# Kernel tuning notes

Hardware: AMD Instinct MI355X
Metric: run time of the kernel (lower is better)

Reference implementation:

```python
import jax, jax.numpy as jnp
import numpy as np


def setup_inputs() -> dict:
    key = jax.random.key(0)
    ks = jax.random.split(key, 4)
    B, S, D, H, E = 2, 2048, 1024, 4096, 8
    scale_in = 1.0 / np.sqrt(D)
    scale_h = 1.0 / np.sqrt(H)
    return {
        "x": jax.random.normal(ks[0], (B, S, D), dtype=jnp.float32),
        "Wr": jax.random.normal(ks[1], (E, D), dtype=jnp.float32) * scale_in,
        "br": jnp.zeros((E,), dtype=jnp.float32),
        "W1": jax.random.normal(ks[2], (E, H, D), dtype=jnp.float32) * scale_in,
        "b1": jnp.zeros((E, H), dtype=jnp.float32),
        "W2": jax.random.normal(ks[3], (E, D, H), dtype=jnp.float32) * scale_h,
        "b2": jnp.zeros((E, D), dtype=jnp.float32),
        "top_k": 2,
    }


def reference(x, Wr, br, W1, b1, W2, b2, top_k):
    B, S, D = x.shape
    E = Wr.shape[0]
    x_flat = x.reshape(-1, D)                                   # [N, D]
    # Router: top-k logits, softmax over the selected k values only
    logits = x_flat @ Wr.T + br                                 # [N, E]
    top_vals, top_idx = jax.lax.top_k(logits, top_k)            # [N, k]
    gates = jax.nn.softmax(top_vals, axis=-1)                   # [N, k]
    # Per-expert combine weight: gate_e[n, e] = sum_k gates[n, k] * 1[top_idx[n,k]==e]
    gate_e = jnp.einsum("nk,nke->ne", gates,
                        jax.nn.one_hot(top_idx, E, dtype=x.dtype))  # [N, E]
    # Dense all-expert MLP (grouped GEMM), then masked combine. Same math as
    # the per-expert gather/scatter loop: unselected experts get zero gate.
    h = jax.nn.relu(jnp.einsum("nd,ehd->neh", x_flat, W1) + b1)     # [N, E, H]
    y = jnp.einsum("neh,edh->ned", h, W2) + b2                      # [N, E, D]
    out = jnp.einsum("ned,ne->nd", y, gate_e)                       # [N, D]
    return out.reshape(B, S, D)
```

## Files before the change

### kernel.cpp

```cpp
#include <hip/hip_runtime.h>
#include <hip/hip_bf16.h>
#include <stdint.h>

#define N_TOK 4096
#define D_ 1024
#define H_ 4096
#define E_ 8
#define NSLOT (N_TOK*2)
#define BM 128
#define BN 128
#define BK 32
#define MAXT 72

typedef __attribute__((ext_vector_type(8))) short short8;
typedef __attribute__((ext_vector_type(4))) float floatx4;
typedef unsigned int u32;

__device__ __forceinline__ unsigned short f2bf(float f){
    union { float f; unsigned int u; } c; c.f = f;
    unsigned int u = c.u;
    unsigned int r = (u + 0x7fffu + ((u >> 16) & 1u)) >> 16;
    return (unsigned short)r;
}

__device__ __forceinline__ void async16(const void* g, void* l){
    __builtin_amdgcn_global_load_lds(
        (const __attribute__((address_space(1))) u32*)g,
        (__attribute__((address_space(3))) u32*)l, 16, 0, 0);
}

__global__ __launch_bounds__(256) void cvt_kernel(
    const float* __restrict__ src, unsigned short* __restrict__ dst, int n4)
{
    int stride = gridDim.x * 256;
    for (int i = blockIdx.x * 256 + threadIdx.x; i < n4; i += stride){
        float4 v = ((const float4*)src)[i];
        ushort4 o; o.x=f2bf(v.x); o.y=f2bf(v.y); o.z=f2bf(v.z); o.w=f2bf(v.w);
        ((ushort4*)dst)[i] = o;
    }
}

__global__ __launch_bounds__(256) void router_kernel(
    const float* __restrict__ x, const float* __restrict__ Wr,
    const float* __restrict__ br, int* __restrict__ topIdx,
    float* __restrict__ topGate)
{
    int n = blockIdx.x * 4 + (threadIdx.x >> 6);
    int lane = threadIdx.x & 63;
    const float4* xp = (const float4*)(x + (size_t)n * D_);
    float acc[E_];
#pragma unroll
    for (int e = 0; e < E_; e++) acc[e] = 0.f;
#pragma unroll
    for (int j = 0; j < 4; j++){
        int idx = j * 64 + lane;
        float4 xv = xp[idx];
#pragma unroll
        for (int e = 0; e < E_; e++){
            float4 wv = ((const float4*)(Wr + (size_t)e * D_))[idx];
            acc[e] += xv.x*wv.x + xv.y*wv.y + xv.z*wv.z + xv.w*wv.w;
        }
    }
#pragma unroll
    for (int e = 0; e < E_; e++){
        float v = acc[e];
        for (int off = 32; off > 0; off >>= 1) v += __shfl_xor(v, off, 64);
        acc[e] = v;
    }
    if (lane == 0){
        float best = -1e30f, second = -1e30f; int bi = 0, si = 0;
#pragma unroll
        for (int e = 0; e < E_; e++){
            float v = acc[e] + br[e];
            if (v > best){ second = best; si = bi; best = v; bi = e; }
            else if (v > second){ second = v; si = e; }
        }
        float e1 = __expf(second - best);
        float denom = 1.f + e1;
        topIdx[n*2+0] = bi;  topIdx[n*2+1] = si;
        topGate[n*2+0] = 1.f/denom;  topGate[n*2+1] = e1/denom;
    }
}

__global__ __launch_bounds__(256) void hist_kernel(
    const int* __restrict__ topIdx, int* __restrict__ hdr)
{
    __shared__ int c[E_];
    int t = threadIdx.x;
    if (t < E_) c[t] = 0;
    __syncthreads();
    int e = topIdx[blockIdx.x * 256 + t];
    atomicAdd(&c[e], 1);
    __syncthreads();
    if (t < E_) hdr[256 + blockIdx.x * E_ + t] = c[t];
}

__global__ __launch_bounds__(64) void scan2_kernel(int* __restrict__ hdr)
{
    __shared__ int cnt[32 * E_];
    __shared__ int tot[E_];
    __shared__ int offs[E_ + 1];
    int t = threadIdx.x;
    for (int i = t; i < 32 * E_; i += 64) cnt[i] = hdr[256 + i];
    __syncthreads();
    if (t < E_){
        int s = 0;
        for (int b = 0; b < 32; b++) s += cnt[b * E_ + t];
        tot[t] = s;
    }
    __syncthreads();
    if (t == 0){
        int o = 0;
        for (int e = 0; e < E_; e++){ offs[e] = o; o += tot[e]; }
        offs[E_] = o;
    }
    __syncthreads();
    if (t < E_ + 1) hdr[16 + t] = offs[t];
    if (t < E_){
        int run = offs[t];
        for (int b = 0; b < 32; b++){ hdr[512 + b * E_ + t] = run; run += cnt[b * E_ + t]; }
    }
    if (t == 0){
        int tn = 0;
        for (int e = 0; e < E_; e++){
            int nt = (tot[e] + BM - 1) >> 7;
            for (int i = 0; i < nt; i++){ hdr[32 + tn] = e; hdr[112 + tn] = offs[e] + (i << 7); tn++; }
        }
        for (; tn < MAXT; tn++){ hdr[32 + tn] = -1; hdr[112 + tn] = 0; }
    }
}

__global__ __launch_bounds__(256) void pos_kernel(
    const int* __restrict__ topIdx, const float* __restrict__ topGate,
    const int* __restrict__ hdr, int* __restrict__ posOf,
    int* __restrict__ rowTok, float* __restrict__ rowGate)
{
    __shared__ int c[E_];
    int t = threadIdx.x;
    if (t < E_) c[t] = 0;
    __syncthreads();
    int slot = blockIdx.x * 256 + t;
    int e = topIdx[slot];
    int r = atomicAdd(&c[e], 1);
    int pos = hdr[512 + blockIdx.x * E_ + e] + r;
    posOf[slot] = pos;
    rowTok[pos] = slot >> 1;
    rowGate[pos] = topGate[slot];
}

__global__ __launch_bounds__(256) void copy_kernel(
    const float* __restrict__ x, const int* __restrict__ posOf,
    unsigned short* __restrict__ xg)
{
    int slot = blockIdx.x * 4 + (threadIdx.x >> 6);
    int lane = threadIdx.x & 63;
    int n = slot >> 1;
    int pos = posOf[slot];
    const float4* xp = (const float4*)(x + (size_t)n * D_);
    ushort4* op = (ushort4*)(xg + (size_t)pos * D_);
#pragma unroll
    for (int j = 0; j < 4; j++){
        float4 v = xp[j * 64 + lane];
        ushort4 o; o.x=f2bf(v.x); o.y=f2bf(v.y); o.z=f2bf(v.z); o.w=f2bf(v.w);
        op[j * 64 + lane] = o;
    }
}

template<int MODE, bool BF16B>
__global__ __launch_bounds__(256) void moe_gemm(
    const unsigned short* __restrict__ A, int Ktot,
    const void* __restrict__ Wbase, size_t wStride,
    const float* __restrict__ biasBase, int biasStride,
    const int* __restrict__ hdr,
    const int* __restrict__ rowTok, const float* __restrict__ rowGate,
    unsigned short* __restrict__ hout, float* __restrict__ out)
{
    int gid = blockIdx.y * gridDim.x + blockIdx.x;
    int per = gridDim.x * 8;
    int g = gid / per, rr = gid % per;
    int by = g * 8 + (rr & 7);
    int bx = rr >> 3;

    int e = hdr[32 + bx];
    if (e < 0) return;
    int rowBase = hdr[112 + bx];
    int validRows = hdr[16 + e + 1] - rowBase;

    int kChunk = Ktot / gridDim.z;
    int kStart = blockIdx.z * kChunk;

    __shared__ __align__(16) unsigned short As[BM * BK];
    __shared__ __align__(16) unsigned short BsH[BF16B ? BN * BK : 1];
    __shared__ __align__(16) float BsF[BF16B ? 1 : BN * BK];

    const float* biasE = biasBase + (size_t)e * biasStride + by * BN;

    const int tid  = threadIdx.x;
    const int lane = tid & 63, wave = tid >> 6;
    const int wm = wave & 1, wn = wave >> 1;
    const int l16 = lane & 15, quad = lane >> 4;

    floatx4 acc[4][4];
#pragma unroll
    for (int mi = 0; mi < 4; mi++)
#pragma unroll
        for (int ni = 0; ni < 4; ni++)
            acc[mi][ni] = (floatx4){0.f,0.f,0.f,0.f};

    int aS[2], aRow[2], aCol[2];
#pragma unroll
    for (int i = 0; i < 2; i++){
        int s = i * 256 + tid;
        aS[i] = s;
        int r = rowBase + (s >> 2);
        aRow[i] = r < (NSLOT - 1) ? r : (NSLOT - 1);
        aCol[i] = (s & 3) * 8;
    }

    if (BF16B){
        const unsigned short* Wexp = (const unsigned short*)Wbase
            + (size_t)e * wStride + (size_t)(by * BN) * Ktot;
        for (int k0 = kStart; k0 < kStart + kChunk; k0 += BK){
#pragma unroll
            for (int i = 0; i < 2; i++)
                async16(A + (size_t)aRow[i] * Ktot + k0 + aCol[i], (char*)As + aS[i] * 16);
#pragma unroll
            for (int i = 0; i < 2; i++){
                int s = i * 256 + tid;
                async16(Wexp + (size_t)(s >> 2) * Ktot + k0 + (s & 3) * 8,
                        (char*)BsH + s * 16);
            }
            __syncthreads();
            short8 af[4], bfr[4];
#pragma unroll
            for (int mi = 0; mi < 4; mi++)
                af[mi] = *(const short8*)(As + (wm*64 + mi*16 + l16) * BK + quad * 8);
#pragma unroll
            for (int ni = 0; ni < 4; ni++)
                bfr[ni] = *(const short8*)(BsH + (wn*64 + ni*16 + l16) * BK + quad * 8);
#pragma unroll
            for (int mi = 0; mi < 4; mi++)
#pragma unroll
                for (int ni = 0; ni < 4; ni++)
                    acc[mi][ni] = __builtin_amdgcn_mfma_f32_16x16x32_bf16(
                        af[mi], bfr[ni], acc[mi][ni], 0, 0, 0);
            __syncthreads();
        }
    } else {
        const float* Wexp = (const float*)Wbase
            + (size_t)e * wStride + (size_t)(by * BN) * Ktot;
        int bS[4], bRow[4], bCol[4];
#pragma unroll
        for (int i = 0; i < 4; i++){
            int s = i * 256 + tid;
            bS[i] = s;
            int r = s >> 3, c = s & 7;
            bRow[i] = r;
            bCol[i] = (c ^ (r & 7)) * 4;
        }
        for (int k0 = kStart; k0 < kStart + kChunk; k0 += BK){
#pragma unroll
            for (int i = 0; i < 2; i++)
                async16(A + (size_t)aRow[i] * Ktot + k0 + aCol[i], (char*)As + aS[i] * 16);
#pragma unroll
            for (int i = 0; i < 4; i++)
                async16(Wexp + (size_t)bRow[i] * Ktot + k0 + bCol[i], (char*)BsF + bS[i] * 16);
            __syncthreads();
            short8 af[4], bfr[4];
#pragma unroll
            for (int mi = 0; mi < 4; mi++)
                af[mi] = *(const short8*)(As + (wm*64 + mi*16 + l16) * BK + quad * 8);
#pragma unroll
            for (int ni = 0; ni < 4; ni++){
                int n = wn*64 + ni*16 + l16;
                int g0 = (2*quad)     ^ (n & 7);
                int g1 = (2*quad + 1) ^ (n & 7);
                float4 u0 = *(const float4*)(BsF + n * BK + g0 * 4);
                float4 u1 = *(const float4*)(BsF + n * BK + g1 * 4);
                union { short8 s; __hip_bfloat162 h[4]; } u;
                u.h[0] = __float22bfloat162_rn(make_float2(u0.x, u0.y));
                u.h[1] = __float22bfloat162_rn(make_float2(u0.z, u0.w));
                u.h[2] = __float22bfloat162_rn(make_float2(u1.x, u1.y));
                u.h[3] = __float22bfloat162_rn(make_float2(u1.z, u1.w));
                bfr[ni] = u.s;
            }
#pragma unroll
            for (int mi = 0; mi < 4; mi++)
#pragma unroll
                for (int ni = 0; ni < 4; ni++)
                    acc[mi][ni] = __builtin_amdgcn_mfma_f32_16x16x32_bf16(
                        af[mi], bfr[ni], acc[mi][ni], 0, 0, 0);
            __syncthreads();
        }
    }

    bool addB = (MODE == 1) || (blockIdx.z == 0);
#pragma unroll
    for (int mi = 0; mi < 4; mi++){
#pragma unroll
        for (int r = 0; r < 4; r++){
            int rl = wm*64 + mi*16 + quad*4 + r;
            if (rl >= validRows) continue;
            int grow = rowBase + rl;
            int   tok  = 0;
            float gate = 0.f;
            if (MODE == 2){ tok = rowTok[grow]; gate = rowGate[grow]; }
#pragma unroll
            for (int ni = 0; ni < 4; ni++){
                int lcol = wn*64 + ni*16 + l16;
                int gcol = by * BN + lcol;
                float v = acc[mi][ni][r] + (addB ? biasE[lcol] : 0.f);
                if (MODE == 1){
                    v = v > 0.f ? v : 0.f;
                    hout[(size_t)grow * H_ + gcol] = f2bf(v);
                } else {
                    atomicAdd(out + (size_t)tok * D_ + gcol, gate * v);
                }
            }
        }
    }
}

extern "C" void kernel_launch(void* const* d_in, const int* in_sizes, int n_in,
                              void* d_out, int out_size, void* d_ws, size_t ws_size,
                              hipStream_t stream)
{
    (void)in_sizes; (void)n_in;
    const float* x  = (const float*)d_in[0];
    const float* Wr = (const float*)d_in[1];
    const float* br = (const float*)d_in[2];
    const float* W1 = (const float*)d_in[3];
    const float* b1 = (const float*)d_in[4];
    const float* W2 = (const float*)d_in[5];
    const float* b2 = (const float*)d_in[6];
    float* out = (float*)d_out;

    char* ws = (char*)d_ws;
    int*   hdr     = (int*)ws;
    int*   topIdx  = (int*)  (ws + 4096);
    float* topGate = (float*)(ws + 36864);
    int*   posOf   = (int*)  (ws + 69632);
    int*   rowTok  = (int*)  (ws + 102400);
    float* rowGate = (float*)(ws + 135168);
    unsigned short* xg   = (unsigned short*)(ws + 262144);
    unsigned short* hbuf = (unsigned short*)(ws + 17039360);
    unsigned short* w1b  = (unsigned short*)(ws + 84148224);
    unsigned short* w2b  = (unsigned short*)(ws + 151257088);
    const bool full = ws_size >= 218365952ull;

    hipMemsetAsync(d_out, 0, (size_t)out_size * sizeof(float), stream);

    router_kernel<<<N_TOK/4, 256, 0, stream>>>(x, Wr, br, topIdx, topGate);
    hist_kernel<<<32, 256, 0, stream>>>(topIdx, hdr);
    scan2_kernel<<<1, 64, 0, stream>>>(hdr);
    pos_kernel<<<32, 256, 0, stream>>>(topIdx, topGate, hdr, posOf, rowTok, rowGate);
    copy_kernel<<<NSLOT/4, 256, 0, stream>>>(x, posOf, xg);

    if (full){
        cvt_kernel<<<2048, 256, 0, stream>>>(W1, w1b, (E_*H_*D_)/4);
        cvt_kernel<<<2048, 256, 0, stream>>>(W2, w2b, (E_*D_*H_)/4);
        moe_gemm<1,true><<<dim3(MAXT, H_/BN, 1), 256, 0, stream>>>(
            xg, D_, w1b, (size_t)H_ * D_, b1, H_, hdr, rowTok, rowGate, hbuf, nullptr);
        moe_gemm<2,true><<<dim3(MAXT, D_/BN, 2), 256, 0, stream>>>(
            hbuf, H_, w2b, (size_t)D_ * H_, b2, D_, hdr, rowTok, rowGate, nullptr, out);
    } else {
        moe_gemm<1,false><<<dim3(MAXT, H_/BN, 1), 256, 0, stream>>>(
            xg, D_, W1, (size_t)H_ * D_, b1, H_, hdr, rowTok, rowGate, hbuf, nullptr);
        moe_gemm<2,false><<<dim3(MAXT, D_/BN, 2), 256, 0, stream>>>(
            hbuf, H_, W2, (size_t)D_ * H_, b2, D_, hdr, rowTok, rowGate, nullptr, out);
    }
}
```

Baseline: 664.4 us.

## Double-buffer bf16 GEMM LDS tiles and XOR-swizzle chunks to avoid bank conflicts

The bf16-weight GEMM path now keeps two LDS stages for the A and B tiles. The next k-slice is prefetched with async global-to-LDS copies while the MFMAs run on the current slice, and only one barrier per iteration remains. The 16-byte chunk position inside each row is also XOR-swizzled by row bits, applied on both store and load, to cut LDS bank conflicts on the short8 fragment reads. This doubles the LDS footprint of that path, which may lower occupancy, and the fp32-weight path is left unpipelined.

```diff
diff --git a/kernel.cpp b/kernel.cpp
--- a/kernel.cpp
+++ b/kernel.cpp
@@ -189,8 +189,8 @@
     int kChunk = Ktot / gridDim.z;
     int kStart = blockIdx.z * kChunk;
 
-    __shared__ __align__(16) unsigned short As[BM * BK];
-    __shared__ __align__(16) unsigned short BsH[BF16B ? BN * BK : 1];
+    __shared__ __align__(16) unsigned short As[2][BM * BK];
+    __shared__ __align__(16) unsigned short BsH[BF16B ? 2 * BN * BK : 1];
     __shared__ __align__(16) float BsF[BF16B ? 1 : BN * BK];
 
     const float* biasE = biasBase + (size_t)e * biasStride + by * BN;
@@ -207,48 +207,74 @@
         for (int ni = 0; ni < 4; ni++)
             acc[mi][ni] = (floatx4){0.f,0.f,0.f,0.f};
 
-    int aS[2], aRow[2], aCol[2];
-#pragma unroll
-    for (int i = 0; i < 2; i++){
-        int s = i * 256 + tid;
-        aS[i] = s;
-        int r = rowBase + (s >> 2);
-        aRow[i] = r < (NSLOT - 1) ? r : (NSLOT - 1);
-        aCol[i] = (s & 3) * 8;
-    }
-
     if (BF16B){
         const unsigned short* Wexp = (const unsigned short*)Wbase
             + (size_t)e * wStride + (size_t)(by * BN) * Ktot;
-        for (int k0 = kStart; k0 < kStart + kChunk; k0 += BK){
-#pragma unroll
-            for (int i = 0; i < 2; i++)
-                async16(A + (size_t)aRow[i] * Ktot + k0 + aCol[i], (char*)As + aS[i] * 16);
-#pragma unroll
-            for (int i = 0; i < 2; i++){
-                int s = i * 256 + tid;
-                async16(Wexp + (size_t)(s >> 2) * Ktot + k0 + (s & 3) * 8,
-                        (char*)BsH + s * 16);
-            }
+
+        size_t aOff[2], bOff[2];
+        int    lOff[2];
+#pragma unroll
+        for (int i = 0; i < 2; i++){
+            int s = i * 256 + tid;
+            int r = s >> 2, gst = s & 3;
+            int gsrc = gst ^ ((r >> 1) & 3);
+            int ar = rowBase + r;
+            ar = ar < (NSLOT - 1) ? ar : (NSLOT - 1);
+            aOff[i] = (size_t)ar * Ktot + gsrc * 8;
+            bOff[i] = (size_t)r  * Ktot + gsrc * 8;
+            lOff[i] = s * 16;
+        }
+
+#pragma unroll
+        for (int i = 0; i < 2; i++){
+            async16(A    + aOff[i] + kStart, (char*)As[0]  + lOff[i]);
+            async16(Wexp + bOff[i] + kStart, (char*)BsH    + lOff[i]);
+        }
+
+        int nIter = kChunk / BK;
+        for (int it = 0; it < nIter; it++){
             __syncthreads();
+            int p = it & 1;
+            if (it + 1 < nIter){
+                int kn = kStart + (it + 1) * BK;
+#pragma unroll
+                for (int i = 0; i < 2; i++){
+                    async16(A    + aOff[i] + kn, (char*)As[p ^ 1] + lOff[i]);
+                    async16(Wexp + bOff[i] + kn, (char*)BsH + (p ^ 1) * (BN * BK * 2) + lOff[i]);
+                }
+            }
             short8 af[4], bfr[4];
 #pragma unroll
-            for (int mi = 0; mi < 4; mi++)
-                af[mi] = *(const short8*)(As + (wm*64 + mi*16 + l16) * BK + quad * 8);
-#pragma unroll
-            for (int ni = 0; ni < 4; ni++)
-                bfr[ni] = *(const short8*)(BsH + (wn*64 + ni*16 + l16) * BK + quad * 8);
+            for (int mi = 0; mi < 4; mi++){
+                int r = wm*64 + mi*16 + l16;
+                int gq = quad ^ ((r >> 1) & 3);
+                af[mi] = *(const short8*)(As[p] + r * BK + gq * 8);
+            }
+#pragma unroll
+            for (int ni = 0; ni < 4; ni++){
+                int n = wn*64 + ni*16 + l16;
+                int gq = quad ^ ((n >> 1) & 3);
+                bfr[ni] = *(const short8*)(BsH + p * (BN * BK) + n * BK + gq * 8);
+            }
 #pragma unroll
             for (int mi = 0; mi < 4; mi++)
 #pragma unroll
                 for (int ni = 0; ni < 4; ni++)
                     acc[mi][ni] = __builtin_amdgcn_mfma_f32_16x16x32_bf16(
                         af[mi], bfr[ni], acc[mi][ni], 0, 0, 0);
-            __syncthreads();
         }
     } else {
         const float* Wexp = (const float*)Wbase
             + (size_t)e * wStride + (size_t)(by * BN) * Ktot;
+        int aS[2], aRow[2], aCol[2];
+#pragma unroll
+        for (int i = 0; i < 2; i++){
+            int s = i * 256 + tid;
+            aS[i] = s;
+            int r = rowBase + (s >> 2);
+            aRow[i] = r < (NSLOT - 1) ? r : (NSLOT - 1);
+            aCol[i] = (s & 3) * 8;
+        }
         int bS[4], bRow[4], bCol[4];
 #pragma unroll
         for (int i = 0; i < 4; i++){
@@ -261,7 +287,7 @@
         for (int k0 = kStart; k0 < kStart + kChunk; k0 += BK){
 #pragma unroll
             for (int i = 0; i < 2; i++)
-                async16(A + (size_t)aRow[i] * Ktot + k0 + aCol[i], (char*)As + aS[i] * 16);
+                async16(A + (size_t)aRow[i] * Ktot + k0 + aCol[i], (char*)As[0] + aS[i] * 16);
 #pragma unroll
             for (int i = 0; i < 4; i++)
                 async16(Wexp + (size_t)bRow[i] * Ktot + k0 + bCol[i], (char*)BsF + bS[i] * 16);
@@ -269,7 +295,7 @@
             short8 af[4], bfr[4];
 #pragma unroll
             for (int mi = 0; mi < 4; mi++)
-                af[mi] = *(const short8*)(As + (wm*64 + mi*16 + l16) * BK + quad * 8);
+                af[mi] = *(const short8*)(As[0] + (wm*64 + mi*16 + l16) * BK + quad * 8);
 #pragma unroll
             for (int ni = 0; ni < 4; ni++){
                 int n = wn*64 + ni*16 + l16;
```

New measurement: 641.4 us. 1.04x faster.
